# Optimization experiments

Measured on AMD Instinct MI355X. Metric: run time of the kernel, lower is better.

## Reference

```python
import jax, jax.numpy as jnp
import numpy as np

V, E, H = 1024, 32, 64
D = 8                     # number of tree levels (root at depth 0)
PER = 149796              # nodes per non-root level
N = 1 + 7 * PER           # 1048573 total nodes


def setup_inputs() -> dict:
    rng = np.random.default_rng(0)
    sizes = [1] + [PER] * (D - 1)
    off = np.concatenate([[0], np.cumsum(sizes)])
    depth = np.repeat(np.arange(D), sizes).astype(np.int64)
    parent = np.zeros(N, dtype=np.int64)  # root points to itself (harmless: its h is 0 when read)
    for l in range(1, D):
        parent[off[l]:off[l + 1]] = rng.integers(off[l - 1], off[l], sizes[l])
    token_ids = rng.integers(0, V, N).astype(np.int64)

    key = jax.random.key(0)
    ks = jax.random.split(key, 7)
    s = 0.05
    return {
        "token_ids": jnp.asarray(token_ids),
        "parent": jnp.asarray(parent),
        "depth": jnp.asarray(depth),
        "max_depth": D - 1,
        "emb": jax.random.normal(ks[0], (V, E), jnp.float32) * s,
        "W_iou_w": jax.random.normal(ks[1], (3 * H, E), jnp.float32) * s,
        "W_iou_b": jax.random.normal(ks[2], (3 * H,), jnp.float32) * s,
        "U_iou_w": jax.random.normal(ks[3], (3 * H, H), jnp.float32) * s,
        "W_f_w": jax.random.normal(ks[4], (H, E), jnp.float32) * s,
        "W_f_b": jax.random.normal(ks[5], (H,), jnp.float32) * s,
        "U_f_w": jax.random.normal(ks[6], (H, H), jnp.float32) * s,
    }


def reference(token_ids, parent, depth, max_depth, emb,
              W_iou_w, W_iou_b, U_iou_w, W_f_w, W_f_b, U_f_w):
    n = token_ids.shape[0]
    hid = U_f_w.shape[0]
    x = emb[token_ids]                                 # [N, E]
    wiou_x = x @ W_iou_w.T + W_iou_b                   # [N, 3H] (input part, precomputed)
    wf_x = x @ W_f_w.T + W_f_b                         # [N, H]
    h = jnp.zeros((n, hid), x.dtype)
    c = jnp.zeros((n, hid), x.dtype)
    # level-synchronous bottom-up sweep (deepest level first); children of a
    # depth-d node are exactly at depth d+1, already finalized when d is processed
    for d in range(max_depth, -1, -1):
        h_sum = jax.ops.segment_sum(h, parent, num_segments=n)        # child-sum per parent
        f = jax.nn.sigmoid(wf_x[parent] + h @ U_f_w.T)                # forget gate per child edge
        fc = jax.ops.segment_sum(f * c, parent, num_segments=n)      # sum_k f_k * c_k per parent
        iou = wiou_x + h_sum @ U_iou_w.T
        i, o, u = jnp.split(iou, 3, axis=-1)
        c_new = jax.nn.sigmoid(i) * jnp.tanh(u) + fc
        h_new = jax.nn.sigmoid(o) * jnp.tanh(c_new)
        m = (depth == d)[:, None]
        h = jnp.where(m, h_new, h)
        c = jnp.where(m, c_new, c)
    return h[0]  # root hidden state, matching TreeLSTMEncoder.forward
```

## Files before the change

kernel.cpp:

```cpp
#include <hip/hip_runtime.h>

#define PER  149796
#define NN   1048573
#define HDIM 64
#define EDIM 32
#define NIOU 192
#define STG  96

typedef _Float16 f16;
typedef _Float16 f16x8 __attribute__((ext_vector_type(8)));
typedef _Float16 f16x4 __attribute__((ext_vector_type(4)));
typedef _Float16 f16x2 __attribute__((ext_vector_type(2)));
typedef float    f32x4 __attribute__((ext_vector_type(4)));

typedef __attribute__((address_space(1))) const unsigned gu32;
typedef __attribute__((address_space(3))) unsigned lu32;

__device__ __forceinline__ float sigf(float x){ return 1.0f/(1.0f+__expf(-x)); }
__device__ __forceinline__ float tanh_f(float x){
  float ax = fabsf(x);
  float e  = __expf(-2.0f*ax);
  float t  = (1.0f - e)/(1.0f + e);
  return x < 0.0f ? -t : t;
}

__global__ __launch_bounds__(256) void countAll_kernel(const int* __restrict__ parent,
                                                       int* __restrict__ cnt){
  int idx = blockIdx.x*256 + threadIdx.x;
  if (idx >= 6*PER) return;
  atomicAdd(&cnt[parent[1 + PER + idx]], 1);
}

__device__ __forceinline__ int cnt_at(const int* cnt, int idx){
  return (idx == 0) ? PER : cnt[idx];
}

__global__ __launch_bounds__(256) void scan1_kernel(const int* __restrict__ cnt, int* __restrict__ bsum){
  __shared__ int sc[256];
  int b = blockIdx.x, t = threadIdx.x;
  int base = b*1024 + t*4;
  int s = 0;
  #pragma unroll
  for (int e=0;e<4;e++){ int idx=base+e; if (idx<NN) s += cnt_at(cnt, idx); }
  sc[t]=s; __syncthreads();
  for (int d=128; d>0; d>>=1){ if (t<d) sc[t]+=sc[t+d]; __syncthreads(); }
  if (t==0) bsum[b]=sc[0];
}

__global__ __launch_bounds__(1024) void scan2_kernel(const int* __restrict__ bsum, int* __restrict__ bbase){
  __shared__ int sc[1024];
  int t=threadIdx.x;
  sc[t]=bsum[t]; __syncthreads();
  for (int d=1; d<1024; d<<=1){
    int v = (t>=d)? sc[t-d] : 0; __syncthreads();
    sc[t]+=v; __syncthreads();
  }
  bbase[t] = (t==0)?0:sc[t-1];
}

__global__ __launch_bounds__(256) void scan3_kernel(const int* __restrict__ cnt, const int* __restrict__ bbase,
                                                    int* __restrict__ off, int* __restrict__ cursor){
  __shared__ int sc[256];
  int b=blockIdx.x, t=threadIdx.x;
  int base=b*1024+t*4;
  int e0 = (base  <NN)?cnt_at(cnt,base  ):0;
  int e1 = (base+1<NN)?cnt_at(cnt,base+1):0;
  int e2 = (base+2<NN)?cnt_at(cnt,base+2):0;
  int e3 = (base+3<NN)?cnt_at(cnt,base+3):0;
  int tsum=e0+e1+e2+e3;
  sc[t]=tsum; __syncthreads();
  for (int d=1; d<256; d<<=1){
    int v=(t>=d)?sc[t-d]:0; __syncthreads();
    sc[t]+=v; __syncthreads();
  }
  int x = bbase[b] + ((t==0)?0:sc[t-1]);
  if (base  <NN){ off[base  ]=x;          cursor[base  ]=x; }
  if (base+1<NN){ off[base+1]=x+e0;       cursor[base+1]=x+e0; }
  if (base+2<NN){ off[base+2]=x+e0+e1;    cursor[base+2]=x+e0+e1; }
  if (base+3<NN){ off[base+3]=x+e0+e1+e2; cursor[base+3]=x+e0+e1+e2; }
}

__global__ __launch_bounds__(256) void scatterAll_kernel(const int* __restrict__ parent,
    const int* __restrict__ tok, int* __restrict__ cursor,
    int* __restrict__ childpos, int* __restrict__ ptok){
  int idx = blockIdx.x*256 + threadIdx.x;
  if (idx >= 6*PER) return;
  int g = 1 + PER + idx;
  int jp = parent[g];
  int pos = atomicAdd(&cursor[jp], 1);
  childpos[g] = pos;
  ptok[pos] = tok[jp];
}

__global__ __launch_bounds__(256) void tablepack_kernel(
    const float* __restrict__ emb, const float* __restrict__ Wiou, const float* __restrict__ biou,
    const float* __restrict__ Wf, const float* __restrict__ bf,
    const float* __restrict__ Uf, const float* __restrict__ Uiou,
    float* __restrict__ embWiou, float* __restrict__ embWf,
    f16* __restrict__ Bfp, f16* __restrict__ Biop)
{
  if (blockIdx.x < 1024){
    int v = blockIdx.x;
    int m = threadIdx.x;
    const float* x = emb + (size_t)v*EDIM;
    if (m < NIOU){
      float a = biou[m];
      #pragma unroll
      for (int e=0;e<EDIM;e++) a += Wiou[m*EDIM+e]*x[e];
      embWiou[(size_t)v*NIOU + m] = a;
    } else {
      int mm = m - NIOU;
      float a = bf[mm];
      #pragma unroll
      for (int e=0;e<EDIM;e++) a += Wf[mm*EDIM+e]*x[e];
      embWf[(size_t)v*HDIM + mm] = a;
    }
  } else {
    for (int i = threadIdx.x; i < 2*4*64*8; i += 256){
      int j = i & 7, L = (i>>3)&63, st = i>>9;
      int t = st & 3, s = st >> 2;
      int k = s*32 + (L>>4)*8 + j;
      int n = t*16 + (L&15);
      Bfp[i] = (f16)Uf[n*HDIM + k];
    }
    for (int i = threadIdx.x; i < 2*12*64*8; i += 256){
      int j = i & 7, L = (i>>3)&63, st = i>>9;
      int t = st % 12, s = st / 12;
      int k = s*32 + (L>>4)*8 + j;
      int n = t*16 + (L&15);
      Biop[i] = (f16)Uiou[n*HDIM + k];
    }
  }
}

__global__ __launch_bounds__(256) void node_fused(
    const int* __restrict__ tok, const int* __restrict__ off,
    const int* __restrict__ childpos, const int* __restrict__ ptok,
    const float* __restrict__ embWiou, const float* __restrict__ embWf,
    const f16* __restrict__ Biopack, const f16* __restrict__ Ufpack,
    const f16x2* __restrict__ HFin, f16x2* __restrict__ HFout,
    int poff, int relbase, int outbase, int identityOut, int leafLevel)
{
  __shared__ __align__(16) char smem[STG*HDIM*4];
  f16x2* stage = (f16x2*)smem;
  f16*   Ah    = (f16*)smem;
  f16*   FAf   = (f16*)(smem + 9216);
  int lane = threadIdx.x & 63;
  int wv   = __builtin_amdgcn_readfirstlane(threadIdx.x >> 6);
  int p0   = wv*16;
  int j0b  = blockIdx.x*64;
  int j0   = j0b + p0;

  float hs[16], fa[16];
  #pragma unroll
  for (int i=0;i<16;i++){ hs[i]=0.f; fa[i]=0.f; }

  if (!leafLevel){
    int ei = j0b + 64; if (ei > PER) ei = PER;
    int S = off[poff + j0b] - relbase;
    int E = off[poff + ei]  - relbase;
    int sB[17];
    #pragma unroll
    for (int i=0;i<=16;i++){
      int jj = j0 + i; if (jj > PER) jj = PER;
      sB[i] = off[poff + jj] - relbase;
    }
    const unsigned* HFinU = (const unsigned*)HFin;
    for (int cb = S; cb < E; cb += STG){
      int n = E - cb; if (n > STG) n = STG;
      for (int r = wv; r < n; r += 4){
        gu32* gp = (gu32*)(HFinU + (size_t)(cb+r)*HDIM) + lane;
        __builtin_amdgcn_global_load_lds(gp, (lu32*)&stage[r*HDIM], 4, 0, 0);
      }
      __syncthreads();
      int lim = cb + n;
      #pragma unroll
      for (int i=0;i<16;i++){
        int lo = sB[i]   > cb  ? sB[i]   : cb;
        int hi = sB[i+1] < lim ? sB[i+1] : lim;
        for (int p=lo; p<hi; ++p){
          f16x2 v = stage[(p-cb)*HDIM + lane];
          hs[i] += (float)v.x; fa[i] += (float)v.y;
        }
      }
      __syncthreads();
    }
  }
  #pragma unroll
  for (int i=0;i<16;i++){
    Ah[(p0+i)*72 + lane]  = (f16)hs[i];
    FAf[(p0+i)*68 + lane] = (f16)fa[i];
  }
  __syncthreads();
  int q = lane>>4, c16 = lane&15;
  f16x8 A0 = *(const f16x8*)(Ah + (p0+c16)*72 + q*8);
  f16x8 A1 = *(const f16x8*)(Ah + (p0+c16)*72 + 32 + q*8);
  const f16x8* Bp = (const f16x8*)Biopack;
  f32x4 acc[12];
  #pragma unroll
  for (int nt=0;nt<12;nt++) acc[nt] = (f32x4){0.f,0.f,0.f,0.f};
  #pragma unroll
  for (int nt=0;nt<12;nt++){
    f16x8 B0 = Bp[nt*64 + lane];
    f16x8 B1 = Bp[(12+nt)*64 + lane];
    acc[nt] = __builtin_amdgcn_mfma_f32_16x16x32_f16(A0, B0, acc[nt], 0,0,0);
    acc[nt] = __builtin_amdgcn_mfma_f32_16x16x32_f16(A1, B1, acc[nt], 0,0,0);
  }
  int tok0 = identityOut ? tok[0] : 0;
  float cc[4][4];
  f16   hh[4][4];
  int   opos_[4]; int wt_[4]; bool ok_[4];
  #pragma unroll
  for (int r=0;r<4;r++){
    int j = j0 + q*4 + r;
    bool ok = j < PER;
    int jl = ok ? j : PER-1;
    int g = poff + jl;
    int tk = tok[g];
    const float* tr = embWiou + (size_t)tk*NIOU;
    int opg = identityOut ? (outbase + jl) : childpos[g];
    int op  = opg - outbase;
    opos_[r]=op; ok_[r]=ok;
    wt_[r] = identityOut ? tok0 : ptok[opg];
    int prow = p0 + q*4 + r;
    #pragma unroll
    for (int nt=0;nt<4;nt++){
      int col = nt*16 + c16;
      float ai = acc[nt][r]   + tr[col];
      float ao = acc[nt+4][r] + tr[64+col];
      float au = acc[nt+8][r] + tr[128+col];
      float fav = (float)FAf[prow*68 + col];
      float c = sigf(ai)*tanh_f(au) + fav;
      float h = sigf(ao)*tanh_f(c);
      cc[r][nt] = c;
      hh[r][nt] = (f16)h;
    }
  }
  __syncthreads();
  #pragma unroll
  for (int r=0;r<4;r++)
    #pragma unroll
    for (int nt=0;nt<4;nt++)
      Ah[(p0+q*4+r)*72 + nt*16 + c16] = hh[r][nt];
  __syncthreads();
  f16x8 H0 = *(const f16x8*)(Ah + (p0+c16)*72 + q*8);
  f16x8 H1 = *(const f16x8*)(Ah + (p0+c16)*72 + 32 + q*8);
  const f16x8* Up = (const f16x8*)Ufpack;
  f32x4 g4[4];
  #pragma unroll
  for (int nt=0;nt<4;nt++) g4[nt] = (f32x4){0.f,0.f,0.f,0.f};
  #pragma unroll
  for (int nt=0;nt<4;nt++){
    f16x8 B0 = Up[nt*64 + lane];
    f16x8 B1 = Up[(4+nt)*64 + lane];
    g4[nt] = __builtin_amdgcn_mfma_f32_16x16x32_f16(H0, B0, g4[nt], 0,0,0);
    g4[nt] = __builtin_amdgcn_mfma_f32_16x16x32_f16(H1, B1, g4[nt], 0,0,0);
  }
  #pragma unroll
  for (int r=0;r<4;r++){
    if (!ok_[r]) continue;
    const float* wr = embWf + (size_t)wt_[r]*HDIM;
    int op = opos_[r];
    #pragma unroll
    for (int nt=0;nt<4;nt++){
      int col = nt*16 + c16;
      float v = sigf(g4[nt][r] + wr[col]) * cc[r][nt];
      f16x2 o; o.x = hh[r][nt]; o.y = (f16)v;
      HFout[(size_t)op*HDIM + col] = o;
    }
  }
}

__global__ __launch_bounds__(256) void rootred_kernel(
    const f16x2* __restrict__ HFin, float* __restrict__ rootacc)
{
  int t = blockIdx.x*blockDim.x + threadIdx.x;
  int m = t & 63;
  int j0 = t >> 6;
  int jstep = (gridDim.x*blockDim.x) >> 6;
  float af=0.f, ah=0.f;
  for (int j=j0; j<PER; j+=jstep){
    f16x2 v = HFin[(size_t)j*HDIM + m];
    ah += (float)v.x;
    af += (float)v.y;
  }
  __shared__ float red[256];
  red[threadIdx.x]=af; __syncthreads();
  if (threadIdx.x < 64) atomicAdd(&rootacc[m],    red[m]+red[64+m]+red[128+m]+red[192+m]);
  __syncthreads();
  red[threadIdx.x]=ah; __syncthreads();
  if (threadIdx.x < 64) atomicAdd(&rootacc[64+m], red[m]+red[64+m]+red[128+m]+red[192+m]);
}

__global__ void rootnode_kernel(
    const int* __restrict__ tok, const float* __restrict__ emb,
    const float* __restrict__ Wiou, const float* __restrict__ biou, const float* __restrict__ Uiou,
    const float* __restrict__ rootacc, float* __restrict__ out)
{
  int m = threadIdx.x;
  if (m >= HDIM) return;
  int t = tok[0];
  float ai=biou[m], ao=biou[HDIM+m], au=biou[2*HDIM+m];
  for (int e=0;e<EDIM;e++){
    float xe = emb[(size_t)t*EDIM+e];
    ai += Wiou[(size_t)m*EDIM+e]*xe;
    ao += Wiou[(size_t)(HDIM+m)*EDIM+e]*xe;
    au += Wiou[(size_t)(2*HDIM+m)*EDIM+e]*xe;
  }
  for (int k=0;k<HDIM;k++){
    float hv = rootacc[64+k];
    ai += Uiou[(size_t)m*HDIM+k]*hv;
    ao += Uiou[(size_t)(HDIM+m)*HDIM+k]*hv;
    au += Uiou[(size_t)(2*HDIM+m)*HDIM+k]*hv;
  }
  float c = sigf(ai)*tanh_f(au) + rootacc[m];
  out[m] = sigf(ao)*tanh_f(c);
}

static inline char* alignup(char* p){
  uintptr_t u = (uintptr_t)p;
  u = (u + 255) & ~(uintptr_t)255;
  return (char*)u;
}

extern "C" void kernel_launch(void* const* d_in, const int* in_sizes, int n_in,
                              void* d_out, int out_size, void* d_ws, size_t ws_size,
                              hipStream_t stream)
{
  const int*   tok    = (const int*)d_in[0];
  const int*   parent = (const int*)d_in[1];
  const float* emb    = (const float*)d_in[4];
  const float* Wiou   = (const float*)d_in[5];
  const float* biou   = (const float*)d_in[6];
  const float* Uiou   = (const float*)d_in[7];
  const float* Wf     = (const float*)d_in[8];
  const float* bf     = (const float*)d_in[9];
  const float* Uf     = (const float*)d_in[10];
  float* out = (float*)d_out;

  char* w = (char*)d_ws;
  f16x2* HFA     = (f16x2*)w;  w = alignup(w + (size_t)PER*HDIM*sizeof(f16x2));
  f16x2* HFB     = (f16x2*)w;  w = alignup(w + (size_t)PER*HDIM*sizeof(f16x2));
  int*   cnt     = (int*)w;    w = alignup(w + (size_t)NN*sizeof(int));
  int*   off     = (int*)w;    w = alignup(w + (size_t)NN*sizeof(int));
  int*   cursor  = (int*)w;    w = alignup(w + (size_t)NN*sizeof(int));
  int*   childpos= (int*)w;    w = alignup(w + (size_t)NN*sizeof(int));
  int*   ptok    = (int*)w;    w = alignup(w + (size_t)NN*sizeof(int));
  int*   bsum    = (int*)w;    w = alignup(w + 1024*sizeof(int));
  int*   bbase   = (int*)w;    w = alignup(w + 1024*sizeof(int));
  float* embWiou = (float*)w;  w = alignup(w + 1024*NIOU*sizeof(float));
  float* embWf   = (float*)w;  w = alignup(w + 1024*HDIM*sizeof(float));
  float* rootacc = (float*)w;  w = alignup(w + 128*sizeof(float));
  f16*   Ufpack  = (f16*)w;    w = alignup(w + 2*4*64*8*sizeof(f16));
  f16*   Biopack = (f16*)w;    w = alignup(w + 2*12*64*8*sizeof(f16));

  const int gALL = (6*PER + 255)/256;

  hipMemsetAsync(cnt, 0, (size_t)(1 + 6*PER)*sizeof(int), stream);
  hipMemsetAsync(rootacc, 0, 128*sizeof(float), stream);

  countAll_kernel  <<<gALL, 256, 0, stream>>>(parent, cnt);
  scan1_kernel     <<<1024, 256, 0, stream>>>(cnt, bsum);
  scan2_kernel     <<<1, 1024, 0, stream>>>(bsum, bbase);
  scan3_kernel     <<<1024, 256, 0, stream>>>(cnt, bbase, off, cursor);
  scatterAll_kernel<<<gALL, 256, 0, stream>>>(parent, tok, cursor, childpos, ptok);
  tablepack_kernel <<<1025, 256, 0, stream>>>(emb, Wiou, biou, Wf, bf, Uf, Uiou,
                                              embWiou, embWf, Ufpack, Biopack);

  f16x2* bufs[2] = {HFA, HFB};
  int outIdx = 0;
  f16x2* last = HFA;
  for (int d=7; d>=1; --d){
    int poff = 1 + (d-1)*PER;
    f16x2* in  = bufs[1-outIdx];
    f16x2* ou  = bufs[outIdx];
    node_fused<<<(PER + 63)/64, 256, 0, stream>>>(tok, off, childpos, ptok,
                                                  embWiou, embWf, Biopack, Ufpack,
                                                  in, ou,
                                                  poff, d*PER, (d-1)*PER,
                                                  (d==1) ? 1 : 0, (d==7) ? 1 : 0);
    last = ou;
    outIdx ^= 1;
  }

  rootred_kernel<<<256, 256, 0, stream>>>(last, rootacc);
  rootnode_kernel<<<1, 64, 0, stream>>>(tok, emb, Wiou, biou, Uiou, rootacc, out);
}
```

Before: 594.7 us.

## Store node outputs in natural order and gather children through a childrow index

Each level's h/f·c outputs are now written at the node's own row, not scattered into child-sorted positions. The child-sum loop instead gathers child rows through a new childrow index array built in the scatter pass. This drops the childpos and ptok arrays and their scattered writes, and the parent token is looked up directly via parent[]. The cost is an indirect index load before each staged row load, and the special root count in the scan is removed.

```diff
diff --git a/kernel.cpp b/kernel.cpp
--- a/kernel.cpp
+++ b/kernel.cpp
@@ -31,17 +31,13 @@
   atomicAdd(&cnt[parent[1 + PER + idx]], 1);
 }
 
-__device__ __forceinline__ int cnt_at(const int* cnt, int idx){
-  return (idx == 0) ? PER : cnt[idx];
-}
-
 __global__ __launch_bounds__(256) void scan1_kernel(const int* __restrict__ cnt, int* __restrict__ bsum){
   __shared__ int sc[256];
   int b = blockIdx.x, t = threadIdx.x;
   int base = b*1024 + t*4;
   int s = 0;
   #pragma unroll
-  for (int e=0;e<4;e++){ int idx=base+e; if (idx<NN) s += cnt_at(cnt, idx); }
+  for (int e=0;e<4;e++){ int idx=base+e; if (idx<NN) s += cnt[idx]; }
   sc[t]=s; __syncthreads();
   for (int d=128; d>0; d>>=1){ if (t<d) sc[t]+=sc[t+d]; __syncthreads(); }
   if (t==0) bsum[b]=sc[0];
@@ -63,10 +59,10 @@
   __shared__ int sc[256];
   int b=blockIdx.x, t=threadIdx.x;
   int base=b*1024+t*4;
-  int e0 = (base  <NN)?cnt_at(cnt,base  ):0;
-  int e1 = (base+1<NN)?cnt_at(cnt,base+1):0;
-  int e2 = (base+2<NN)?cnt_at(cnt,base+2):0;
-  int e3 = (base+3<NN)?cnt_at(cnt,base+3):0;
+  int e0 = (base  <NN)?cnt[base  ]:0;
+  int e1 = (base+1<NN)?cnt[base+1]:0;
+  int e2 = (base+2<NN)?cnt[base+2]:0;
+  int e3 = (base+3<NN)?cnt[base+3]:0;
   int tsum=e0+e1+e2+e3;
   sc[t]=tsum; __syncthreads();
   for (int d=1; d<256; d<<=1){
@@ -81,15 +77,13 @@
 }
 
 __global__ __launch_bounds__(256) void scatterAll_kernel(const int* __restrict__ parent,
-    const int* __restrict__ tok, int* __restrict__ cursor,
-    int* __restrict__ childpos, int* __restrict__ ptok){
+    int* __restrict__ cursor, int* __restrict__ childrow){
   int idx = blockIdx.x*256 + threadIdx.x;
   if (idx >= 6*PER) return;
   int g = 1 + PER + idx;
   int jp = parent[g];
   int pos = atomicAdd(&cursor[jp], 1);
-  childpos[g] = pos;
-  ptok[pos] = tok[jp];
+  childrow[pos] = idx % PER;
 }
 
 __global__ __launch_bounds__(256) void tablepack_kernel(
@@ -134,12 +128,12 @@
 }
 
 __global__ __launch_bounds__(256) void node_fused(
-    const int* __restrict__ tok, const int* __restrict__ off,
-    const int* __restrict__ childpos, const int* __restrict__ ptok,
+    const int* __restrict__ tok, const int* __restrict__ parent,
+    const int* __restrict__ off, const int* __restrict__ childrow,
     const float* __restrict__ embWiou, const float* __restrict__ embWf,
     const f16* __restrict__ Biopack, const f16* __restrict__ Ufpack,
     const f16x2* __restrict__ HFin, f16x2* __restrict__ HFout,
-    int poff, int relbase, int outbase, int identityOut, int leafLevel)
+    int poff, int leafLevel)
 {
   __shared__ __align__(16) char smem[STG*HDIM*4];
   f16x2* stage = (f16x2*)smem;
@@ -157,19 +151,20 @@
 
   if (!leafLevel){
     int ei = j0b + 64; if (ei > PER) ei = PER;
-    int S = off[poff + j0b] - relbase;
-    int E = off[poff + ei]  - relbase;
+    int S = off[poff + j0b];
+    int E = off[poff + ei];
     int sB[17];
     #pragma unroll
     for (int i=0;i<=16;i++){
       int jj = j0 + i; if (jj > PER) jj = PER;
-      sB[i] = off[poff + jj] - relbase;
+      sB[i] = off[poff + jj];
     }
     const unsigned* HFinU = (const unsigned*)HFin;
     for (int cb = S; cb < E; cb += STG){
       int n = E - cb; if (n > STG) n = STG;
       for (int r = wv; r < n; r += 4){
-        gu32* gp = (gu32*)(HFinU + (size_t)(cb+r)*HDIM) + lane;
+        int srow = childrow[cb + r];
+        gu32* gp = (gu32*)(HFinU + (size_t)srow*HDIM) + lane;
         __builtin_amdgcn_global_load_lds(gp, (lu32*)&stage[r*HDIM], 4, 0, 0);
       }
       __syncthreads();
@@ -206,10 +201,9 @@
     acc[nt] = __builtin_amdgcn_mfma_f32_16x16x32_f16(A0, B0, acc[nt], 0,0,0);
     acc[nt] = __builtin_amdgcn_mfma_f32_16x16x32_f16(A1, B1, acc[nt], 0,0,0);
   }
-  int tok0 = identityOut ? tok[0] : 0;
   float cc[4][4];
   f16   hh[4][4];
-  int   opos_[4]; int wt_[4]; bool ok_[4];
+  int   wt_[4]; bool ok_[4];
   #pragma unroll
   for (int r=0;r<4;r++){
     int j = j0 + q*4 + r;
@@ -218,10 +212,8 @@
     int g = poff + jl;
     int tk = tok[g];
     const float* tr = embWiou + (size_t)tk*NIOU;
-    int opg = identityOut ? (outbase + jl) : childpos[g];
-    int op  = opg - outbase;
-    opos_[r]=op; ok_[r]=ok;
-    wt_[r] = identityOut ? tok0 : ptok[opg];
+    wt_[r] = tok[parent[g]];
+    ok_[r] = ok;
     int prow = p0 + q*4 + r;
     #pragma unroll
     for (int nt=0;nt<4;nt++){
@@ -260,13 +252,13 @@
   for (int r=0;r<4;r++){
     if (!ok_[r]) continue;
     const float* wr = embWf + (size_t)wt_[r]*HDIM;
-    int op = opos_[r];
+    int j = j0 + q*4 + r;
     #pragma unroll
     for (int nt=0;nt<4;nt++){
       int col = nt*16 + c16;
       float v = sigf(g4[nt][r] + wr[col]) * cc[r][nt];
       f16x2 o; o.x = hh[r][nt]; o.y = (f16)v;
-      HFout[(size_t)op*HDIM + col] = o;
+      HFout[(size_t)j*HDIM + col] = o;
     }
   }
 }
@@ -344,8 +336,7 @@
   int*   cnt     = (int*)w;    w = alignup(w + (size_t)NN*sizeof(int));
   int*   off     = (int*)w;    w = alignup(w + (size_t)NN*sizeof(int));
   int*   cursor  = (int*)w;    w = alignup(w + (size_t)NN*sizeof(int));
-  int*   childpos= (int*)w;    w = alignup(w + (size_t)NN*sizeof(int));
-  int*   ptok    = (int*)w;    w = alignup(w + (size_t)NN*sizeof(int));
+  int*   childrow= (int*)w;    w = alignup(w + ((size_t)6*PER + 256)*sizeof(int));
   int*   bsum    = (int*)w;    w = alignup(w + 1024*sizeof(int));
   int*   bbase   = (int*)w;    w = alignup(w + 1024*sizeof(int));
   float* embWiou = (float*)w;  w = alignup(w + 1024*NIOU*sizeof(float));
@@ -363,7 +354,7 @@
   scan1_kernel     <<<1024, 256, 0, stream>>>(cnt, bsum);
   scan2_kernel     <<<1, 1024, 0, stream>>>(bsum, bbase);
   scan3_kernel     <<<1024, 256, 0, stream>>>(cnt, bbase, off, cursor);
-  scatterAll_kernel<<<gALL, 256, 0, stream>>>(parent, tok, cursor, childpos, ptok);
+  scatterAll_kernel<<<gALL, 256, 0, stream>>>(parent, cursor, childrow);
   tablepack_kernel <<<1025, 256, 0, stream>>>(emb, Wiou, biou, Wf, bf, Uf, Uiou,
                                               embWiou, embWf, Ufpack, Biopack);
 
@@ -374,11 +365,9 @@
     int poff = 1 + (d-1)*PER;
     f16x2* in  = bufs[1-outIdx];
     f16x2* ou  = bufs[outIdx];
-    node_fused<<<(PER + 63)/64, 256, 0, stream>>>(tok, off, childpos, ptok,
+    node_fused<<<(PER + 63)/64, 256, 0, stream>>>(tok, parent, off, childrow,
                                                   embWiou, embWf, Biopack, Ufpack,
-                                                  in, ou,
-                                                  poff, d*PER, (d-1)*PER,
-                                                  (d==1) ? 1 : 0, (d==7) ? 1 : 0);
+                                                  in, ou, poff, (d==7) ? 1 : 0);
     last = ou;
     outIdx ^= 1;
   }
```

Result: faster. 553.6 us (-6.9%).
